# Performance work log

Measured on AMD Instinct MI355X. Metric: run time of the kernel, lower is better.

Reference implementation:

```python
import jax, jax.numpy as jnp
import numpy as np

# bitsandbytes NF4 codebook (16 quantile values in [-1, 1])
NF4 = jnp.array([
    -1.0, -0.6961928009986877, -0.5250730514526367, -0.39491748809814453,
    -0.28444138169288635, -0.18477343022823334, -0.09105003625154495, 0.0,
    0.07958029955625534, 0.16093020141124725, 0.24611230194568634,
    0.33791524171829224, 0.44070982933044434, 0.5626170039176941,
    0.7229568362236328, 1.0], dtype=jnp.float32)
BLOCK = 64  # bnb default quantization blocksize


def dequant_nf4(codes, absmax):
    """codes: int array of 4-bit indices, absmax: per-64-elem-block scale."""
    flat = NF4[codes.reshape(-1)]                      # codebook lookup
    flat = flat.reshape(-1, BLOCK) * absmax[:, None]   # per-block rescale
    return flat.reshape(codes.shape)


def setup_inputs() -> dict:
    key = jax.random.key(0)
    k1, k2, k3, k4, k5 = jax.random.split(key, 5)
    B, S, IN, OUT, R = 4, 2048, 4096, 4096, 8
    x = jax.random.normal(k1, (B, S, IN), dtype=jnp.float32)
    codes_A = jax.random.randint(k2, (R, IN), 0, 16, dtype=jnp.int32)
    absmax_A = jax.random.uniform(k3, (R * IN // BLOCK,), dtype=jnp.float32)
    codes_B = jax.random.randint(k4, (OUT, R), 0, 16, dtype=jnp.int32)
    absmax_B = jax.random.uniform(k5, (OUT * R // BLOCK,), dtype=jnp.float32)
    return {"x": x, "codes_A": codes_A, "absmax_A": absmax_A,
            "codes_B": codes_B, "absmax_B": absmax_B}


def reference(x, codes_A, absmax_A, codes_B, absmax_B):
    SCALING = 32.0 / 8.0  # alpha / rank
    W_A = dequant_nf4(codes_A, absmax_A)   # [rank, in]
    W_B = dequant_nf4(codes_B, absmax_B)   # [out, rank]
    interm = jnp.einsum('bsi,ri->bsr', x, W_A)          # lora_A: x @ W_A^T
    out = jnp.einsum('bsr,or->bso', interm, W_B)        # lora_B
    return out * SCALING
```

## Files before the change

### kernel.cpp

```cpp
#include <hip/hip_runtime.h>


static __device__ __constant__ float NF4_TBL[16] = {
    -1.0f, -0.6961928009986877f, -0.5250730514526367f, -0.39491748809814453f,
    -0.28444138169288635f, -0.18477343022823334f, -0.09105003625154495f, 0.0f,
    0.07958029955625534f, 0.16093020141124725f, 0.24611230194568634f,
    0.33791524171829224f, 0.44070982933044434f, 0.5626170039176941f,
    0.7229568362236328f, 1.0f};

__global__ void nf4_dequant_kernel(const int* __restrict__ codesA,
                                   const float* __restrict__ absA,
                                   const int* __restrict__ codesB,
                                   const float* __restrict__ absB,
                                   float* __restrict__ wA,
                                   float* __restrict__ wB,
                                   int n) {
    int id = blockIdx.x * blockDim.x + threadIdx.x;
    if (id < n) {
        wA[id] = NF4_TBL[codesA[id] & 15] * absA[id >> 6];
        wB[id] = NF4_TBL[codesB[id] & 15] * absB[id >> 6];
    }
}

__global__ __launch_bounds__(256, 4) void qlora_fused_kernel(
    const float* __restrict__ x,
    const float* __restrict__ wA,
    const float* __restrict__ wB,
    float* __restrict__ out) {
    constexpr int IN = 4096;
    constexpr int OUT = 4096;
    constexpr int ROWS = 8;

    __shared__ float interm[ROWS][8];

    const int t    = threadIdx.x;
    const int wave = t >> 6;
    const int lane = t & 63;
    const int row0 = blockIdx.x * ROWS;

    {
        const int r0 = row0 + 2 * wave;
        const float4* __restrict__ x0  = (const float4*)(x + (size_t)r0 * IN);
        const float4* __restrict__ x1  = (const float4*)(x + (size_t)(r0 + 1) * IN);
        const float4* __restrict__ wA4 = (const float4*)wA;

        float acc0[8], acc1[8];
        #pragma unroll
        for (int r = 0; r < 8; ++r) { acc0[r] = 0.f; acc1[r] = 0.f; }

        #pragma unroll 4
        for (int c = 0; c < IN / 4 / 64; ++c) {
            const int idx = lane + 64 * c;
            const float4 xa = x0[idx];
            const float4 xb = x1[idx];
            #pragma unroll
            for (int r = 0; r < 8; ++r) {
                const float4 w = wA4[r * (IN / 4) + idx];
                acc0[r] += xa.x * w.x + xa.y * w.y + xa.z * w.z + xa.w * w.w;
                acc1[r] += xb.x * w.x + xb.y * w.y + xb.z * w.z + xb.w * w.w;
            }
        }

        #pragma unroll
        for (int r = 0; r < 8; ++r) {
            float v0 = acc0[r], v1 = acc1[r];
            #pragma unroll
            for (int off = 32; off > 0; off >>= 1) {
                v0 += __shfl_down(v0, off, 64);
                v1 += __shfl_down(v1, off, 64);
            }
            if (lane == 0) {
                interm[2 * wave + 0][r] = v0 * 4.0f;
                interm[2 * wave + 1][r] = v1 * 4.0f;
            }
        }
    }
    __syncthreads();

    const float4* __restrict__ wB4 = (const float4*)wB;
    #pragma unroll
    for (int k = 0; k < 4; ++k) {
        const int og = t + 256 * k;
        float4 wrow[8];
        #pragma unroll
        for (int j = 0; j < 8; ++j) wrow[j] = wB4[8 * og + j];

        #pragma unroll
        for (int m = 0; m < ROWS; ++m) {
            const float4 i0 = ((const float4*)interm[m])[0];
            const float4 i1 = ((const float4*)interm[m])[1];
            float4 s;
            s.x = i0.x * wrow[0].x + i0.y * wrow[0].y + i0.z * wrow[0].z + i0.w * wrow[0].w
                + i1.x * wrow[1].x + i1.y * wrow[1].y + i1.z * wrow[1].z + i1.w * wrow[1].w;
            s.y = i0.x * wrow[2].x + i0.y * wrow[2].y + i0.z * wrow[2].z + i0.w * wrow[2].w
                + i1.x * wrow[3].x + i1.y * wrow[3].y + i1.z * wrow[3].z + i1.w * wrow[3].w;
            s.z = i0.x * wrow[4].x + i0.y * wrow[4].y + i0.z * wrow[4].z + i0.w * wrow[4].w
                + i1.x * wrow[5].x + i1.y * wrow[5].y + i1.z * wrow[5].z + i1.w * wrow[5].w;
            s.w = i0.x * wrow[6].x + i0.y * wrow[6].y + i0.z * wrow[6].z + i0.w * wrow[6].w
                + i1.x * wrow[7].x + i1.y * wrow[7].y + i1.z * wrow[7].z + i1.w * wrow[7].w;
            ((float4*)(out + (size_t)(row0 + m) * OUT))[og] = s;
        }
    }
}

extern "C" void kernel_launch(void* const* d_in, const int* in_sizes, int n_in,
                              void* d_out, int out_size, void* d_ws, size_t ws_size,
                              hipStream_t stream) {
    const float* x       = (const float*)d_in[0];
    const int*   codes_A = (const int*)d_in[1];
    const float* absmax_A= (const float*)d_in[2];
    const int*   codes_B = (const int*)d_in[3];
    const float* absmax_B= (const float*)d_in[4];
    float* out = (float*)d_out;

    constexpr int NW = 8 * 4096;
    float* wA = (float*)d_ws;
    float* wB = (float*)d_ws + NW;

    nf4_dequant_kernel<<<(NW + 255) / 256, 256, 0, stream>>>(
        codes_A, absmax_A, codes_B, absmax_B, wA, wB, NW);

    const int n_rows = 4 * 2048;
    qlora_fused_kernel<<<n_rows / 8, 256, 0, stream>>>(x, wA, wB, out);
}
```

Baseline: 283.4 us.

## Split IN across waves with 8-row register tile and butterfly transpose-reduce

Each wave now covers a quarter of the input columns for all 8 rows, instead of two rows across the full width. Each loaded W_A float4 is reused across 8 rows rather than 2, which cuts W_A reload traffic. The 64 per-lane accumulators are reduced with a recursive-halving shfl_xor butterfly that leaves one (row, rank) sum per lane, then combined across waves through shared memory. The cost is 64 accumulator registers per thread, which puts pressure on occupancy at launch_bounds(256,4), plus an extra barrier.

Result: slower. 341.9 us (+20.6%).

```diff
diff --git a/kernel.cpp b/kernel.cpp
--- a/kernel.cpp
+++ b/kernel.cpp
@@ -27,11 +27,11 @@
     const float* __restrict__ wA,
     const float* __restrict__ wB,
     float* __restrict__ out) {
-    constexpr int IN = 4096;
-    constexpr int OUT = 4096;
+    constexpr int IN4  = 4096 / 4;
     constexpr int ROWS = 8;
 
-    __shared__ float interm[ROWS][8];
+    __shared__ float  partial[4][64];
+    __shared__ float4 interm4[ROWS][2];
 
     const int t    = threadIdx.x;
     const int wave = t >> 6;
@@ -39,41 +39,53 @@
     const int row0 = blockIdx.x * ROWS;
 
     {
-        const int r0 = row0 + 2 * wave;
-        const float4* __restrict__ x0  = (const float4*)(x + (size_t)r0 * IN);
-        const float4* __restrict__ x1  = (const float4*)(x + (size_t)(r0 + 1) * IN);
+        const float4* __restrict__ x4  = (const float4*)x + (size_t)row0 * IN4;
         const float4* __restrict__ wA4 = (const float4*)wA;
+        const int colbase = wave * 256;
 
-        float acc0[8], acc1[8];
+        float acc[64];
         #pragma unroll
-        for (int r = 0; r < 8; ++r) { acc0[r] = 0.f; acc1[r] = 0.f; }
+        for (int i = 0; i < 64; ++i) acc[i] = 0.f;
 
-        #pragma unroll 4
-        for (int c = 0; c < IN / 4 / 64; ++c) {
-            const int idx = lane + 64 * c;
-            const float4 xa = x0[idx];
-            const float4 xb = x1[idx];
+        #pragma unroll
+        for (int c = 0; c < 4; ++c) {
+            const int idx = colbase + 64 * c + lane;
+            float4 w[8];
             #pragma unroll
-            for (int r = 0; r < 8; ++r) {
-                const float4 w = wA4[r * (IN / 4) + idx];
-                acc0[r] += xa.x * w.x + xa.y * w.y + xa.z * w.z + xa.w * w.w;
-                acc1[r] += xb.x * w.x + xb.y * w.y + xb.z * w.z + xb.w * w.w;
+            for (int r = 0; r < 8; ++r) w[r] = wA4[r * IN4 + idx];
+            #pragma unroll
+            for (int row = 0; row < ROWS; ++row) {
+                const float4 xa = x4[row * IN4 + idx];
+                #pragma unroll
+                for (int r = 0; r < 8; ++r)
+                    acc[row * 8 + r] += xa.x * w[r].x + xa.y * w[r].y
+                                      + xa.z * w[r].z + xa.w * w[r].w;
             }
         }
 
         #pragma unroll
-        for (int r = 0; r < 8; ++r) {
-            float v0 = acc0[r], v1 = acc1[r];
+        for (int s = 0; s < 6; ++s) {
+            const int d  = 1 << s;
+            const int cnt = 32 >> s;
+            const bool kb = (lane & d) != 0;
             #pragma unroll
-            for (int off = 32; off > 0; off >>= 1) {
-                v0 += __shfl_down(v0, off, 64);
-                v1 += __shfl_down(v1, off, 64);
-            }
-            if (lane == 0) {
-                interm[2 * wave + 0][r] = v0 * 4.0f;
-                interm[2 * wave + 1][r] = v1 * 4.0f;
+            for (int j = 0; j < 32; ++j) {
+                if (j < cnt) {
+                    const float a0 = acc[2 * j];
+                    const float a1 = acc[2 * j + 1];
+                    const float keep = kb ? a1 : a0;
+                    const float send = kb ? a0 : a1;
+                    acc[j] = keep + __shfl_xor(send, d, 64);
+                }
             }
         }
+        partial[wave][lane] = acc[0];
+    }
+    __syncthreads();
+    if (wave == 0) {
+        const float s = partial[0][lane] + partial[1][lane]
+                      + partial[2][lane] + partial[3][lane];
+        ((float*)interm4)[lane] = s * 4.0f;
     }
     __syncthreads();
 
@@ -87,8 +99,8 @@
 
         #pragma unroll
         for (int m = 0; m < ROWS; ++m) {
-            const float4 i0 = ((const float4*)interm[m])[0];
-            const float4 i1 = ((const float4*)interm[m])[1];
+            const float4 i0 = interm4[m][0];
+            const float4 i1 = interm4[m][1];
             float4 s;
             s.x = i0.x * wrow[0].x + i0.y * wrow[0].y + i0.z * wrow[0].z + i0.w * wrow[0].w
                 + i1.x * wrow[1].x + i1.y * wrow[1].y + i1.z * wrow[1].z + i1.w * wrow[1].w;
@@ -98,7 +110,7 @@
                 + i1.x * wrow[5].x + i1.y * wrow[5].y + i1.z * wrow[5].z + i1.w * wrow[5].w;
             s.w = i0.x * wrow[6].x + i0.y * wrow[6].y + i0.z * wrow[6].z + i0.w * wrow[6].w
                 + i1.x * wrow[7].x + i1.y * wrow[7].y + i1.z * wrow[7].z + i1.w * wrow[7].w;
-            ((float4*)(out + (size_t)(row0 + m) * OUT))[og] = s;
+            ((float4*)(out + (size_t)(row0 + m) * 4096))[og] = s;
         }
     }
 }
@@ -106,11 +118,11 @@
 extern "C" void kernel_launch(void* const* d_in, const int* in_sizes, int n_in,
                               void* d_out, int out_size, void* d_ws, size_t ws_size,
                               hipStream_t stream) {
-    const float* x       = (const float*)d_in[0];
-    const int*   codes_A = (const int*)d_in[1];
-    const float* absmax_A= (const float*)d_in[2];
-    const int*   codes_B = (const int*)d_in[3];
-    const float* absmax_B= (const float*)d_in[4];
+    const float* x        = (const float*)d_in[0];
+    const int*   codes_A  = (const int*)d_in[1];
+    const float* absmax_A = (const float*)d_in[2];
+    const int*   codes_B  = (const int*)d_in[3];
+    const float* absmax_B = (const float*)d_in[4];
     float* out = (float*)d_out;
 
     constexpr int NW = 8 * 4096;
```

## Split fused LoRA kernel into A and B passes with transposed W_B

Applied to the files above, without the earlier changes.

Separates the fused kernel into a lora_A reduction kernel that writes the rank-8 intermediate to workspace and a lora_B expansion kernel. The dequant step now stores W_B transposed so that B-phase weight loads are coalesced across threads. The goal is to remove the in-block barrier between the reduction and output phases and let each phase run at its own occupancy. The cost is an extra kernel launch and a small global round trip for the intermediate.

Measured after the change: 257.6 us. -9.1%, faster.

```diff
diff --git a/kernel.cpp b/kernel.cpp
--- a/kernel.cpp
+++ b/kernel.cpp
@@ -13,92 +13,104 @@
                                    const int* __restrict__ codesB,
                                    const float* __restrict__ absB,
                                    float* __restrict__ wA,
-                                   float* __restrict__ wB,
+                                   float* __restrict__ wBt,
                                    int n) {
     int id = blockIdx.x * blockDim.x + threadIdx.x;
     if (id < n) {
         wA[id] = NF4_TBL[codesA[id] & 15] * absA[id >> 6];
-        wB[id] = NF4_TBL[codesB[id] & 15] * absB[id >> 6];
+        const int o = id >> 3;
+        const int r = id & 7;
+        wBt[r * 4096 + o] = NF4_TBL[codesB[id] & 15] * absB[id >> 6];
     }
 }
 
-__global__ __launch_bounds__(256, 4) void qlora_fused_kernel(
+__global__ __launch_bounds__(256, 4) void lora_a_kernel(
     const float* __restrict__ x,
     const float* __restrict__ wA,
-    const float* __restrict__ wB,
-    float* __restrict__ out) {
-    constexpr int IN = 4096;
-    constexpr int OUT = 4096;
-    constexpr int ROWS = 8;
-
-    __shared__ float interm[ROWS][8];
+    float* __restrict__ interm) {
+    constexpr int IN4 = 4096 / 4;
 
     const int t    = threadIdx.x;
     const int wave = t >> 6;
     const int lane = t & 63;
-    const int row0 = blockIdx.x * ROWS;
+    const int r0   = blockIdx.x * 8 + 2 * wave;
 
-    {
-        const int r0 = row0 + 2 * wave;
-        const float4* __restrict__ x0  = (const float4*)(x + (size_t)r0 * IN);
-        const float4* __restrict__ x1  = (const float4*)(x + (size_t)(r0 + 1) * IN);
-        const float4* __restrict__ wA4 = (const float4*)wA;
+    const float4* __restrict__ x0  = (const float4*)(x + (size_t)r0 * 4096);
+    const float4* __restrict__ x1  = (const float4*)(x + (size_t)(r0 + 1) * 4096);
+    const float4* __restrict__ wA4 = (const float4*)wA;
 
-        float acc0[8], acc1[8];
-        #pragma unroll
-        for (int r = 0; r < 8; ++r) { acc0[r] = 0.f; acc1[r] = 0.f; }
+    float acc0[8], acc1[8];
+    #pragma unroll
+    for (int r = 0; r < 8; ++r) { acc0[r] = 0.f; acc1[r] = 0.f; }
 
-        #pragma unroll 4
-        for (int c = 0; c < IN / 4 / 64; ++c) {
-            const int idx = lane + 64 * c;
-            const float4 xa = x0[idx];
-            const float4 xb = x1[idx];
-            #pragma unroll
-            for (int r = 0; r < 8; ++r) {
-                const float4 w = wA4[r * (IN / 4) + idx];
-                acc0[r] += xa.x * w.x + xa.y * w.y + xa.z * w.z + xa.w * w.w;
-                acc1[r] += xb.x * w.x + xb.y * w.y + xb.z * w.z + xb.w * w.w;
-            }
-        }
-
+    #pragma unroll 4
+    for (int c = 0; c < 16; ++c) {
+        const int idx = lane + 64 * c;
+        const float4 xa = x0[idx];
+        const float4 xb = x1[idx];
         #pragma unroll
         for (int r = 0; r < 8; ++r) {
-            float v0 = acc0[r], v1 = acc1[r];
-            #pragma unroll
-            for (int off = 32; off > 0; off >>= 1) {
-                v0 += __shfl_down(v0, off, 64);
-                v1 += __shfl_down(v1, off, 64);
-            }
-            if (lane == 0) {
-                interm[2 * wave + 0][r] = v0 * 4.0f;
-                interm[2 * wave + 1][r] = v1 * 4.0f;
-            }
+            const float4 w = wA4[r * IN4 + idx];
+            acc0[r] += xa.x * w.x + xa.y * w.y + xa.z * w.z + xa.w * w.w;
+            acc1[r] += xb.x * w.x + xb.y * w.y + xb.z * w.z + xb.w * w.w;
         }
     }
-    __syncthreads();
 
-    const float4* __restrict__ wB4 = (const float4*)wB;
+    #pragma unroll
+    for (int r = 0; r < 8; ++r) {
+        float v0 = acc0[r], v1 = acc1[r];
+        #pragma unroll
+        for (int off = 32; off > 0; off >>= 1) {
+            v0 += __shfl_down(v0, off, 64);
+            v1 += __shfl_down(v1, off, 64);
+        }
+        if (lane == 0) {
+            interm[(size_t)r0 * 8 + r]       = v0 * 4.0f;
+            interm[(size_t)(r0 + 1) * 8 + r] = v1 * 4.0f;
+        }
+    }
+}
+
+__global__ __launch_bounds__(256, 8) void lora_b_kernel(
+    const float* __restrict__ interm,
+    const float* __restrict__ wBt,
+    float* __restrict__ out) {
+    const int t    = threadIdx.x;
+    const int row0 = blockIdx.x * 4;
+
+    float im[4][8];
+    const float* __restrict__ ip = interm + (size_t)row0 * 8;
+    #pragma unroll
+    for (int m = 0; m < 4; ++m)
+        #pragma unroll
+        for (int r = 0; r < 8; ++r)
+            im[m][r] = ip[m * 8 + r];
+
+    const float4* __restrict__ wt = (const float4*)wBt;
+
     #pragma unroll
     for (int k = 0; k < 4; ++k) {
         const int og = t + 256 * k;
-        float4 wrow[8];
+        float4 w[8];
         #pragma unroll
-        for (int j = 0; j < 8; ++j) wrow[j] = wB4[8 * og + j];
+        for (int r = 0; r < 8; ++r) w[r] = wt[r * 1024 + og];
 
         #pragma unroll
-        for (int m = 0; m < ROWS; ++m) {
-            const float4 i0 = ((const float4*)interm[m])[0];
-            const float4 i1 = ((const float4*)interm[m])[1];
+        for (int m = 0; m < 4; ++m) {
             float4 s;
-            s.x = i0.x * wrow[0].x + i0.y * wrow[0].y + i0.z * wrow[0].z + i0.w * wrow[0].w
-                + i1.x * wrow[1].x + i1.y * wrow[1].y + i1.z * wrow[1].z + i1.w * wrow[1].w;
-            s.y = i0.x * wrow[2].x + i0.y * wrow[2].y + i0.z * wrow[2].z + i0.w * wrow[2].w
-                + i1.x * wrow[3].x + i1.y * wrow[3].y + i1.z * wrow[3].z + i1.w * wrow[3].w;
-            s.z = i0.x * wrow[4].x + i0.y * wrow[4].y + i0.z * wrow[4].z + i0.w * wrow[4].w
-                + i1.x * wrow[5].x + i1.y * wrow[5].y + i1.z * wrow[5].z + i1.w * wrow[5].w;
-            s.w = i0.x * wrow[6].x + i0.y * wrow[6].y + i0.z * wrow[6].z + i0.w * wrow[6].w
-                + i1.x * wrow[7].x + i1.y * wrow[7].y + i1.z * wrow[7].z + i1.w * wrow[7].w;
-            ((float4*)(out + (size_t)(row0 + m) * OUT))[og] = s;
+            s.x = im[m][0] * w[0].x + im[m][1] * w[1].x + im[m][2] * w[2].x
+                + im[m][3] * w[3].x + im[m][4] * w[4].x + im[m][5] * w[5].x
+                + im[m][6] * w[6].x + im[m][7] * w[7].x;
+            s.y = im[m][0] * w[0].y + im[m][1] * w[1].y + im[m][2] * w[2].y
+                + im[m][3] * w[3].y + im[m][4] * w[4].y + im[m][5] * w[5].y
+                + im[m][6] * w[6].y + im[m][7] * w[7].y;
+            s.z = im[m][0] * w[0].z + im[m][1] * w[1].z + im[m][2] * w[2].z
+                + im[m][3] * w[3].z + im[m][4] * w[4].z + im[m][5] * w[5].z
+                + im[m][6] * w[6].z + im[m][7] * w[7].z;
+            s.w = im[m][0] * w[0].w + im[m][1] * w[1].w + im[m][2] * w[2].w
+                + im[m][3] * w[3].w + im[m][4] * w[4].w + im[m][5] * w[5].w
+                + im[m][6] * w[6].w + im[m][7] * w[7].w;
+            ((float4*)(out + (size_t)(row0 + m) * 4096))[og] = s;
         }
     }
 }
@@ -106,20 +118,21 @@
 extern "C" void kernel_launch(void* const* d_in, const int* in_sizes, int n_in,
                               void* d_out, int out_size, void* d_ws, size_t ws_size,
                               hipStream_t stream) {
-    const float* x       = (const float*)d_in[0];
-    const int*   codes_A = (const int*)d_in[1];
-    const float* absmax_A= (const float*)d_in[2];
-    const int*   codes_B = (const int*)d_in[3];
-    const float* absmax_B= (const float*)d_in[4];
+    const float* x        = (const float*)d_in[0];
+    const int*   codes_A  = (const int*)d_in[1];
+    const float* absmax_A = (const float*)d_in[2];
+    const int*   codes_B  = (const int*)d_in[3];
+    const float* absmax_B = (const float*)d_in[4];
     float* out = (float*)d_out;
 
     constexpr int NW = 8 * 4096;
-    float* wA = (float*)d_ws;
-    float* wB = (float*)d_ws + NW;
+    float* wA     = (float*)d_ws;
+    float* wBt    = (float*)d_ws + NW;
+    float* interm = (float*)d_ws + 2 * NW;
 
     nf4_dequant_kernel<<<(NW + 255) / 256, 256, 0, stream>>>(
-        codes_A, absmax_A, codes_B, absmax_B, wA, wB, NW);
+        codes_A, absmax_A, codes_B, absmax_B, wA, wBt, NW);
 
-    const int n_rows = 4 * 2048;
-    qlora_fused_kernel<<<n_rows / 8, 256, 0, stream>>>(x, wA, wB, out);
+    lora_a_kernel<<<8192 / 8, 256, 0, stream>>>(x, wA, interm);
+    lora_b_kernel<<<8192 / 4, 256, 0, stream>>>(interm, wBt, out);
 }
```
